# Optimization experiments

Hardware: AMD Instinct MI355X
Metric: run time of the kernel (lower is better)

The kernel has to match this reference:

```python
import jax, jax.numpy as jnp
import numpy as np

T, B, V, D, H, L, AH = 64, 128, 50000, 300, 300, 20, 300
EPS = 1e-8


def lstm_scan(x, Wih, Whh, b, h_dim):
    # x: [T, N, d_in]; PyTorch LSTM gate order i, f, g, o
    N = x.shape[1]

    def step(carry, xt):
        h, c = carry
        g = xt @ Wih.T + h @ Whh.T + b
        i, f, gg, o = jnp.split(g, 4, axis=-1)
        c = jax.nn.sigmoid(f) * c + jax.nn.sigmoid(i) * jnp.tanh(gg)
        h = jax.nn.sigmoid(o) * jnp.tanh(c)
        return (h, c), h

    init = (jnp.zeros((N, h_dim), x.dtype), jnp.zeros((N, h_dim), x.dtype))
    _, hs = jax.lax.scan(step, init, x)
    return hs  # [T, N, h_dim]


def mp_full(p, v, W):
    # p:[T,B,H], v:[B,H], W:[L,H] -> [T,B,L]; cos(W_l*p, W_l*v) via W^2 contraction
    W2 = W * W
    num = jnp.einsum('tbh,bh,lh->tbl', p, v, W2)
    pn = jnp.sqrt(jnp.einsum('tbh,lh->tbl', p * p, W2))
    vn = jnp.sqrt(jnp.einsum('bh,lh->bl', v * v, W2))
    return num / (pn * vn[None] + EPS)


def mp_elem(p, q, W):
    # p,q:[T,B,H] -> [T,B,L]
    W2 = W * W
    num = jnp.einsum('tbh,lh->tbl', p * q, W2)
    pn = jnp.sqrt(jnp.einsum('tbh,lh->tbl', p * p, W2))
    qn = jnp.sqrt(jnp.einsum('tbh,lh->tbl', q * q, W2))
    return num / (pn * qn + EPS)


def mp_pair(p, h, W):
    # p:[Tp,B,H], h:[Th,B,H] -> [Tp,Th,B,L]
    W2 = W * W
    num = jnp.einsum('tbh,sbh,lh->tsbl', p, h, W2)
    pn = jnp.sqrt(jnp.einsum('tbh,lh->tbl', p * p, W2))
    hn = jnp.sqrt(jnp.einsum('sbh,lh->sbl', h * h, W2))
    return num / (pn[:, None] * hn[None] + EPS)


def match_dir(p, h, v_full, Wf, Wm, Wa, Wma):
    full = mp_full(p, v_full, Wf)                       # full matching
    maxp = mp_pair(p, h, Wm).max(axis=1)                # maxpooling matching
    pn = p / (jnp.linalg.norm(p, axis=-1, keepdims=True) + EPS)
    hn = h / (jnp.linalg.norm(h, axis=-1, keepdims=True) + EPS)
    att = jnp.einsum('tbh,sbh->tsb', pn, hn)            # cosine attention
    w = att / (att.sum(axis=1, keepdims=True) + EPS)
    hmean = jnp.einsum('tsb,sbh->tbh', w, h)
    attm = mp_elem(p, hmean, Wa)                        # attentive matching
    idx = jnp.argmax(att, axis=1)                       # [Tp,B]
    hmax = h[idx, jnp.arange(h.shape[1])]               # [Tp,B,H]
    maxattm = mp_elem(p, hmax, Wma)                     # max-attentive matching
    return jnp.concatenate([full, maxp, attm, maxattm], axis=-1)


def multi_perspective(p_fw, p_bw, h_fw, h_bw, mp_W):
    m_fw = match_dir(p_fw, h_fw, h_fw[-1], mp_W[0], mp_W[1], mp_W[2], mp_W[3])
    m_bw = match_dir(p_bw, h_bw, h_bw[0], mp_W[4], mp_W[5], mp_W[6], mp_W[7])
    return jnp.concatenate([m_fw, m_bw], axis=-1)  # [T,B,8L]


def setup_inputs() -> dict:
    key = jax.random.key(0)
    ks = jax.random.split(key, 20)
    s = 0.05
    return {
        'premise': jax.random.randint(ks[0], (T, B), 0, V),
        'hypothesis': jax.random.randint(ks[1], (T, B), 0, V),
        'embed_W': jax.random.normal(ks[2], (V, D), jnp.float32),
        'cell_Wih': jax.random.normal(ks[3], (4 * H, D), jnp.float32) * s,
        'cell_Whh': jax.random.normal(ks[4], (4 * H, H), jnp.float32) * s,
        'cell_b': jax.random.normal(ks[5], (4 * H,), jnp.float32) * s,
        'mp_W': jax.random.normal(ks[6], (8, L, H), jnp.float32),
        'agg_Wih_f': jax.random.normal(ks[7], (4 * AH, 16 * L), jnp.float32) * s,
        'agg_Whh_f': jax.random.normal(ks[8], (4 * AH, AH), jnp.float32) * s,
        'agg_b_f': jax.random.normal(ks[9], (4 * AH,), jnp.float32) * s,
        'agg_Wih_b': jax.random.normal(ks[10], (4 * AH, 16 * L), jnp.float32) * s,
        'agg_Whh_b': jax.random.normal(ks[11], (4 * AH, AH), jnp.float32) * s,
        'agg_b_b': jax.random.normal(ks[12], (4 * AH,), jnp.float32) * s,
        'bn_gamma': jnp.ones((3, 2 * AH), jnp.float32),
        'bn_beta': jnp.zeros((3, 2 * AH), jnp.float32),
        'mlp_W1': jax.random.normal(ks[13], (2 * AH, 2 * AH), jnp.float32) * s,
        'mlp_b1': jax.random.normal(ks[14], (2 * AH,), jnp.float32) * s,
        'mlp_W2': jax.random.normal(ks[15], (2 * AH, 2 * AH), jnp.float32) * s,
        'mlp_b2': jax.random.normal(ks[16], (2 * AH,), jnp.float32) * s,
        'out_W': jax.random.normal(ks[17], (3, 2 * AH), jnp.float32) * s,
        'out_b': jax.random.normal(ks[18], (3,), jnp.float32) * s,
    }


def reference(premise, hypothesis, embed_W, cell_Wih, cell_Whh, cell_b, mp_W,
              agg_Wih_f, agg_Whh_f, agg_b_f, agg_Wih_b, agg_Whh_b, agg_b_b,
              bn_gamma, bn_beta, mlp_W1, mlp_b1, mlp_W2, mlp_b2, out_W, out_b):
    p = embed_W[premise]                      # [T,B,D]
    h = embed_W[hypothesis]                   # [T,B,D]
    comb = jnp.concatenate([p, h], axis=1)    # [T,2B,D] (premise|hypothesis along batch)
    hs_fw = lstm_scan(comb, cell_Wih, cell_Whh, cell_b, H)
    hs_bw = lstm_scan(comb[::-1], cell_Wih, cell_Whh, cell_b, H)[::-1]  # time-aligned
    p_fw, h_fw = hs_fw[:, :B], hs_fw[:, B:]
    p_bw, h_bw = hs_bw[:, :B], hs_bw[:, B:]
    m_ph = multi_perspective(p_fw, p_bw, h_fw, h_bw, mp_W)
    m_hp = multi_perspective(h_fw, h_bw, p_fw, p_bw, mp_W)
    m = jnp.concatenate([m_ph, m_hp], axis=-1)  # [T,B,16L]
    a_f = lstm_scan(m, agg_Wih_f, agg_Whh_f, agg_b_f, AH)[-1]
    a_b = lstm_scan(m[::-1], agg_Wih_b, agg_Whh_b, agg_b_b, AH)[-1]
    x = jnp.concatenate([a_f, a_b], axis=-1)    # [B, 2*AH]
    inv = np.float32(1.0 / np.sqrt(1.0 + 1e-5))  # eval-mode BN, running stats (0,1)
    bn = lambda z, i: bn_gamma[i] * z * inv + bn_beta[i]
    x = jax.nn.relu(bn(x, 0) @ mlp_W1.T + mlp_b1)
    x = jax.nn.relu(bn(x, 1) @ mlp_W2.T + mlp_b2)
    return bn(x, 2) @ out_W.T + out_b           # [B, 3]
```

## Files before the change

kernel.cpp:

```cpp
#include <hip/hip_runtime.h>
#include <cstddef>
#include <cstdint>
#include <math.h>

#define EPSF 1e-8f


typedef _Float16 half8v __attribute__((ext_vector_type(8)));
typedef float f32x4v __attribute__((ext_vector_type(4)));
union U4H8 { uint4 u; half8v h; _Float16 e[8]; };

__device__ __forceinline__ float fsig(float x) {
  float e = __expf(-x);
  return __builtin_amdgcn_rcpf(1.f + e);
}
__device__ __forceinline__ float ftanh(float x) {
  float e = __expf(-2.f * fabsf(x));
  float r = (1.f - e) * __builtin_amdgcn_rcpf(1.f + e);
  return copysignf(r, x);
}

__device__ __forceinline__ uint4 gld16(const uint4* p) {
  uint4 r;
  asm volatile("global_load_dwordx4 %0, %1, off" : "=v"(r) : "v"(p));
  return r;
}

__global__ __launch_bounds__(256) void gemm_nt128(
    const float* __restrict__ A, const float* __restrict__ B,
    const float* __restrict__ bias, float* __restrict__ C,
    int M, int N, int K)
{
  __shared__ float As[16][128];
  __shared__ float Bs[16][128];
  const int tid = threadIdx.x;
  const int tx = tid & 15, ty = tid >> 4;
  const int mbase = blockIdx.y << 7, nbase = blockIdx.x << 7;
  const int lm = tid >> 1;
  const int lk = (tid & 1) << 3;
  float acc[8][8];
#pragma unroll
  for (int i = 0; i < 8; i++)
#pragma unroll
    for (int j = 0; j < 8; j++) acc[i][j] = 0.f;

  for (int kk = 0; kk < K; kk += 16) {
    {
      int m = mbase + lm;
      const float* src = A + (size_t)m * K;
#pragma unroll
      for (int q = 0; q < 2; q++) {
        int kb = kk + lk + q * 4;
        float4 v = make_float4(0.f, 0.f, 0.f, 0.f);
        if (m < M) {
          if (kb + 4 <= K) {
            v = *(const float4*)(src + kb);
          } else {
            v.x = (kb + 0 < K) ? src[kb + 0] : 0.f;
            v.y = (kb + 1 < K) ? src[kb + 1] : 0.f;
            v.z = (kb + 2 < K) ? src[kb + 2] : 0.f;
            v.w = (kb + 3 < K) ? src[kb + 3] : 0.f;
          }
        }
        As[lk + q * 4 + 0][lm] = v.x;
        As[lk + q * 4 + 1][lm] = v.y;
        As[lk + q * 4 + 2][lm] = v.z;
        As[lk + q * 4 + 3][lm] = v.w;
      }
    }
    {
      int n = nbase + lm;
      const float* src = B + (size_t)n * K;
#pragma unroll
      for (int q = 0; q < 2; q++) {
        int kb = kk + lk + q * 4;
        float4 v = make_float4(0.f, 0.f, 0.f, 0.f);
        if (n < N) {
          if (kb + 4 <= K) {
            v = *(const float4*)(src + kb);
          } else {
            v.x = (kb + 0 < K) ? src[kb + 0] : 0.f;
            v.y = (kb + 1 < K) ? src[kb + 1] : 0.f;
            v.z = (kb + 2 < K) ? src[kb + 2] : 0.f;
            v.w = (kb + 3 < K) ? src[kb + 3] : 0.f;
          }
        }
        Bs[lk + q * 4 + 0][lm] = v.x;
        Bs[lk + q * 4 + 1][lm] = v.y;
        Bs[lk + q * 4 + 2][lm] = v.z;
        Bs[lk + q * 4 + 3][lm] = v.w;
      }
    }
    __syncthreads();
#pragma unroll
    for (int k = 0; k < 16; k++) {
      float4 a0 = *(const float4*)&As[k][ty * 8];
      float4 a1 = *(const float4*)&As[k][ty * 8 + 4];
      float4 b0 = *(const float4*)&Bs[k][tx * 8];
      float4 b1 = *(const float4*)&Bs[k][tx * 8 + 4];
      float av[8] = {a0.x, a0.y, a0.z, a0.w, a1.x, a1.y, a1.z, a1.w};
      float bv[8] = {b0.x, b0.y, b0.z, b0.w, b1.x, b1.y, b1.z, b1.w};
#pragma unroll
      for (int i = 0; i < 8; i++)
#pragma unroll
        for (int j = 0; j < 8; j++) acc[i][j] += av[i] * bv[j];
    }
    __syncthreads();
  }

#pragma unroll
  for (int i = 0; i < 8; i++) {
    int m = mbase + ty * 8 + i;
    if (m >= M) continue;
#pragma unroll
    for (int jq = 0; jq < 2; jq++) {
      int n = nbase + tx * 8 + jq * 4;
      if (n >= N) continue;
      float4 v = make_float4(acc[i][jq * 4], acc[i][jq * 4 + 1],
                             acc[i][jq * 4 + 2], acc[i][jq * 4 + 3]);
      if (bias) {
        v.x += bias[n]; v.y += bias[n + 1]; v.z += bias[n + 2]; v.w += bias[n + 3];
      }
      *(float4*)(C + (size_t)m * N + n) = v;
    }
  }
}

__global__ __launch_bounds__(256) void permW_kernel(
    const float* __restrict__ W, const float* __restrict__ bias,
    float* __restrict__ Wp, float* __restrict__ bp, int K)
{
  int r = blockIdx.x;
  int gate = r & 3, u = r >> 2;
  int src = gate * 300 + u;
  const float* s = W + (size_t)src * K;
  float* d = Wp + (size_t)r * K;
  for (int c = threadIdx.x; c < K; c += 256) d[c] = s[c];
  if (threadIdx.x == 0) bp[r] = bias[src];
}

__global__ __launch_bounds__(256) void packB_kernel(
    const float* __restrict__ W0, const float* __restrict__ W1,
    const float* __restrict__ W2,
    uint4* __restrict__ T0, uint4* __restrict__ T1, uint4* __restrict__ T2)
{
  int i = blockIdx.x * 256 + threadIdx.x;
  if (i >= 48000) return;
  const float* W = (blockIdx.y == 0) ? W0 : (blockIdx.y == 1) ? W1 : W2;
  uint4* T = (blockIdx.y == 0) ? T0 : (blockIdx.y == 1) ? T1 : T2;
  int lane = i & 63;
  int tile = i >> 6;
  int nt = tile / 10, kt = tile - nt * 10;
  int lm = lane & 15, lg = lane >> 4;
  int colp = nt * 16 + lm;
  int u = colp >> 2, gate = colp & 3;
  int n = gate * 300 + u;
  U4H8 v;
#pragma unroll
  for (int j = 0; j < 8; j++) {
    int k = kt * 32 + lg * 8 + j;
    float x = (k < 300) ? W[(size_t)n * 300 + k] : 0.f;
    v.e[j] = (_Float16)x;
  }
  T[i] = v.u;
}

#define LSTM_LDS_BYTES (5248 + 38528 + 11 * 10240)

__global__ __launch_bounds__(512, 2) void lstm_res(
    const uint4* WB0, const uint4* WB1,
    const float* __restrict__ gx0, const float* __restrict__ gx1,
    float* hist0, float* hist1,
    float* hfin,
    int NB)
{
  extern __shared__ char smem[];
  _Float16* hA8 = (_Float16*)smem;
  float* gsh = (float*)(smem + 5248);
  uint4* bls = (uint4*)(smem + 5248 + 38528);

  const int b = blockIdx.x;
  const int xcd = b & 7;
  const int grp = b >> 3;
  const int dirb = xcd >> 2;
  const int n0 = (grp * 4 + (xcd & 3)) * 8;
  const int tid = threadIdx.x;
  const int wv = tid >> 6, lane = tid & 63;
  const int lm = lane & 15, lg = lane >> 4;

  const uint4* WB = dirb ? WB1 : WB0;
  const float* gx = dirb ? gx1 : gx0;
  float* hist = dirb ? hist1 : hist0;

  U4H8 br0[10], br1[10];
  {
    const uint4* p0 = WB + (size_t)(wv * 10) * 64 + lane;
    const uint4* p1 = WB + (size_t)((wv + 8) * 10) * 64 + lane;
#pragma unroll
    for (int kt = 0; kt < 10; kt++) br0[kt].u = gld16(p0 + kt * 64);
#pragma unroll
    for (int kt = 0; kt < 10; kt++) br1[kt].u = gld16(p1 + kt * 64);
  }
  for (int e = tid; e < 7040; e += 512) bls[e] = WB[16 * 640 + e];
  for (int e = tid; e < 8 * 328; e += 512) hA8[e] = (_Float16)0.f;
  asm volatile("s_waitcnt vmcnt(0)" ::: "memory");
  __builtin_amdgcn_sched_barrier(0);
  __syncthreads();

  int gxo[5], gsho[5], hAo[5], ho[5];
  bool act[5];
#pragma unroll
  for (int q = 0; q < 5; q++) {
    int e = tid + q * 512;
    act[q] = (e < 2400);
    int m = act[q] ? (e / 300) : 0;
    int u = act[q] ? (e - m * 300) : 0;
    gxo[q] = (n0 + m) * 1200 + 4 * u;
    gsho[q] = m * 1204 + 4 * u;
    hAo[q] = m * 328 + u;
    ho[q] = (n0 + m) * 300 + u;
  }

  float crs[5] = {0.f, 0.f, 0.f, 0.f, 0.f};

  for (int t = 0; t < 64; t++) {
    const int tg = dirb ? (63 - t) : t;
    const size_t gxstep = (size_t)tg * NB * 1200;

    float4 gxv[5];
#pragma unroll
    for (int q = 0; q < 5; q++) {
      gxv[q] = make_float4(0.f, 0.f, 0.f, 0.f);
      if (act[q]) gxv[q] = *(const float4*)(gx + gxstep + gxo[q]);
    }

    uint4 bA[5], bB[5];
#pragma unroll
    for (int kt = 0; kt < 5; kt++)
      bA[kt] = WB[(size_t)((27 + wv) * 10 + kt) * 64 + lane];

    U4H8 af[10];
#pragma unroll
    for (int kt = 0; kt < 10; kt++) {
      uint4 v = make_uint4(0u, 0u, 0u, 0u);
      if (lm < 8) v = *(const uint4*)&hA8[lm * 328 + kt * 32 + lg * 8];
      af[kt].u = v;
    }

    {
      f32x4v a0 = {0.f, 0.f, 0.f, 0.f};
      f32x4v a1 = {0.f, 0.f, 0.f, 0.f};
#pragma unroll
      for (int kt = 0; kt < 5; kt++)
        a0 = __builtin_amdgcn_mfma_f32_16x16x32_f16(af[kt].h, br0[kt].h, a0, 0, 0, 0);
#pragma unroll
      for (int kt = 5; kt < 10; kt++)
        a1 = __builtin_amdgcn_mfma_f32_16x16x32_f16(af[kt].h, br0[kt].h, a1, 0, 0, 0);
      if (lg < 2) {
        int col = wv * 16 + lm;
#pragma unroll
        for (int r = 0; r < 4; r++)
          gsh[(lg * 4 + r) * 1204 + col] = a0[r] + a1[r];
      }
    }
    {
      f32x4v a0 = {0.f, 0.f, 0.f, 0.f};
      f32x4v a1 = {0.f, 0.f, 0.f, 0.f};
#pragma unroll
      for (int kt = 0; kt < 5; kt++)
        a0 = __builtin_amdgcn_mfma_f32_16x16x32_f16(af[kt].h, br1[kt].h, a0, 0, 0, 0);
#pragma unroll
      for (int kt = 5; kt < 10; kt++)
        a1 = __builtin_amdgcn_mfma_f32_16x16x32_f16(af[kt].h, br1[kt].h, a1, 0, 0, 0);
      if (lg < 2) {
        int col = (wv + 8) * 16 + lm;
#pragma unroll
        for (int r = 0; r < 4; r++)
          gsh[(lg * 4 + r) * 1204 + col] = a0[r] + a1[r];
      }
    }

#pragma unroll 1
    for (int i = 0; i < 6; i++) {
      int nt = 27 + wv + 8 * i;
#pragma unroll
      for (int kt = 0; kt < 5; kt++)
        bB[kt] = WB[(size_t)(nt * 10 + 5 + kt) * 64 + lane];
      f32x4v a0 = {0.f, 0.f, 0.f, 0.f};
#pragma unroll
      for (int kt = 0; kt < 5; kt++) {
        U4H8 bb; bb.u = bA[kt];
        a0 = __builtin_amdgcn_mfma_f32_16x16x32_f16(af[kt].h, bb.h, a0, 0, 0, 0);
      }
      if (i + 1 < 6) {
#pragma unroll
        for (int kt = 0; kt < 5; kt++)
          bA[kt] = WB[(size_t)((nt + 8) * 10 + kt) * 64 + lane];
      }
      f32x4v a1 = {0.f, 0.f, 0.f, 0.f};
#pragma unroll
      for (int kt = 0; kt < 5; kt++) {
        U4H8 bb; bb.u = bB[kt];
        a1 = __builtin_amdgcn_mfma_f32_16x16x32_f16(af[5 + kt].h, bb.h, a1, 0, 0, 0);
      }
      if (lg < 2) {
        int col = nt * 16 + lm;
#pragma unroll
        for (int r = 0; r < 4; r++)
          gsh[(lg * 4 + r) * 1204 + col] = a0[r] + a1[r];
      }
    }

#pragma unroll 1
    for (int li = 0; li < 2; li++) {
      int idxL = li == 0 ? wv : (8 + wv);
      if (li == 1 && wv >= 3) break;
      const uint4* bt = &bls[idxL * 640];
      f32x4v a0 = {0.f, 0.f, 0.f, 0.f};
      f32x4v a1 = {0.f, 0.f, 0.f, 0.f};
#pragma unroll
      for (int kt = 0; kt < 5; kt++) {
        U4H8 bb; bb.u = bt[kt * 64 + lane];
        a0 = __builtin_amdgcn_mfma_f32_16x16x32_f16(af[kt].h, bb.h, a0, 0, 0, 0);
      }
#pragma unroll
      for (int kt = 5; kt < 10; kt++) {
        U4H8 bb; bb.u = bt[kt * 64 + lane];
        a1 = __builtin_amdgcn_mfma_f32_16x16x32_f16(af[kt].h, bb.h, a1, 0, 0, 0);
      }
      if (lg < 2) {
        int col = (16 + idxL) * 16 + lm;
#pragma unroll
        for (int r = 0; r < 4; r++)
          gsh[(lg * 4 + r) * 1204 + col] = a0[r] + a1[r];
      }
    }
    __syncthreads();

#pragma unroll
    for (int q = 0; q < 5; q++) {
      if (act[q]) {
        const float4 gs = *(const float4*)&gsh[gsho[q]];
        float gi = gxv[q].x + gs.x;
        float gf = gxv[q].y + gs.y;
        float gg = gxv[q].z + gs.z;
        float go = gxv[q].w + gs.w;
        float si = fsig(gi);
        float sf = fsig(gf);
        float so = fsig(go);
        float cc = sf * crs[q] + si * ftanh(gg);
        float h = so * ftanh(cc);
        crs[q] = cc;
        hA8[hAo[q]] = (_Float16)h;
        if (hist) hist[(size_t)tg * NB * 300 + ho[q]] = h;
        if (hfin && t == 63) hfin[(size_t)dirb * NB * 300 + ho[q]] = h;
      }
    }
    __syncthreads();
  }
}

__global__ void embed_kernel(
    const int* __restrict__ prem, const int* __restrict__ hyp,
    const float* __restrict__ embW, float* __restrict__ comb)
{
  size_t i = (size_t)blockIdx.x * 256 + threadIdx.x;
  if (i >= (size_t)64 * 256 * 75) return;
  int d4 = (int)(i % 75);
  size_t r = i / 75;
  int n = (int)(r % 256);
  int t = (int)(r / 256);
  int id = (n < 128) ? prem[t * 128 + n] : hyp[t * 128 + (n - 128)];
  float4 v = *(const float4*)(embW + (size_t)id * 300 + d4 * 4);
  *(float4*)(comb + ((size_t)t * 256 + n) * 300 + d4 * 4) = v;
}

__global__ __launch_bounds__(320) void norm4_kernel(
    const float* __restrict__ hs_fw, const float* __restrict__ hs_bw,
    const float* __restrict__ mp_W,
    float* __restrict__ nm4, float* __restrict__ pnorm)
{
  const int t = blockIdx.x, n = blockIdx.y, dir = blockIdx.z;
  const float* HS = dir ? hs_bw : hs_fw;
  const float* row = HS + ((size_t)t * 256 + n) * 300;
  __shared__ float sh[300];
  const int tid = threadIdx.x, g = tid >> 4, lane = tid & 15;
  for (int k = tid; k < 300; k += 320) sh[k] = row[k];
  __syncthreads();
  if (g == 0) {
    float s2 = 0.f;
    for (int k = lane; k < 300; k += 16) { float x = sh[k]; s2 += x * x; }
    for (int o = 8; o; o >>= 1) s2 += __shfl_down(s2, o, 16);
    if (lane == 0) pnorm[((size_t)dir * 64 + t) * 256 + n] = sqrtf(s2);
  }
#pragma unroll
  for (int wset = 0; wset < 4; wset++) {
    const float* W = mp_W + dir * 24000 + wset * 6000 + g * 300;
    float s1 = 0.f;
    for (int k = lane; k < 300; k += 16) {
      float x = sh[k];
      float w = W[k];
      s1 += x * x * w * w;
    }
    for (int o = 8; o; o >>= 1) s1 += __shfl_down(s1, o, 16);
    if (lane == 0)
      nm4[((((size_t)dir * 4 + wset) * 64 + t) * 256 + n) * 20 + g] = sqrtf(s1);
  }
}

__global__ __launch_bounds__(256) void att_kernel(
    const float* __restrict__ hs_fw, const float* __restrict__ hs_bw,
    const float* __restrict__ pnorm,
    float* __restrict__ watt, int* __restrict__ idxbuf)
{
  const int b = blockIdx.x, z = blockIdx.y;
  const int dir = z & 1;
  const float* HS = dir ? hs_bw : hs_fw;
  const int p_n = (z < 2) ? b : 128 + b;
  const int h_n = (z < 2) ? 128 + b : b;
  const float* pnD = pnorm + (size_t)dir * 16384;

  __shared__ float pch[64 * 100];
  __shared__ float hch[64 * 100];
  __shared__ float att[64 * 65];
  __shared__ float winv_sh[64];

  const int tid = threadIdx.x;
  const int i = tid >> 4, j = tid & 15;
  float acc[4][4];
#pragma unroll
  for (int a = 0; a < 4; a++)
#pragma unroll
    for (int c = 0; c < 4; c++) acc[a][c] = 0.f;

  for (int kc = 0; kc < 300; kc += 100) {
    for (int e = tid; e < 1600; e += 256) {
      int row = e / 25, kq = e - row * 25;
      float4 v = *(const float4*)(HS + ((size_t)row * 256 + p_n) * 300 + kc + kq * 4);
      *(float4*)&pch[row * 100 + kq * 4] = v;
      float4 w = *(const float4*)(HS + ((size_t)row * 256 + h_n) * 300 + kc + kq * 4);
      *(float4*)&hch[row * 100 + kq * 4] = w;
    }
    __syncthreads();
#pragma unroll 5
    for (int kq = 0; kq < 25; kq++) {
      float4 av[4], bv[4];
#pragma unroll
      for (int a = 0; a < 4; a++) av[a] = *(const float4*)&pch[(i + 16 * a) * 100 + kq * 4];
#pragma unroll
      for (int c = 0; c < 4; c++) bv[c] = *(const float4*)&hch[(j + 16 * c) * 100 + kq * 4];
#pragma unroll
      for (int a = 0; a < 4; a++)
#pragma unroll
        for (int c = 0; c < 4; c++)
          acc[a][c] += av[a].x * bv[c].x + av[a].y * bv[c].y + av[a].z * bv[c].z + av[a].w * bv[c].w;
    }
    __syncthreads();
  }

#pragma unroll
  for (int a = 0; a < 4; a++) {
    int t = i + 16 * a;
    float pn = pnD[t * 256 + p_n] + EPSF;
#pragma unroll
    for (int c = 0; c < 4; c++) {
      int s = j + 16 * c;
      float hn = pnD[s * 256 + h_n] + EPSF;
      att[t * 65 + s] = acc[a][c] / (pn * hn);
    }
  }
  __syncthreads();
  if (tid < 64) {
    int t = tid;
    float ssum = 0.f, mx = -1e30f; int mi = 0;
    for (int s = 0; s < 64; s++) {
      float a = att[t * 65 + s];
      ssum += a;
      if (a > mx) { mx = a; mi = s; }
    }
    winv_sh[t] = 1.f / (ssum + EPSF);
    idxbuf[((size_t)z * 128 + b) * 64 + t] = mi;
  }
  __syncthreads();
  for (int e = tid; e < 4096; e += 256) {
    int t = e >> 6, s = e & 63;
    watt[((size_t)z * 128 + b) * 4096 + t * 64 + s] = att[t * 65 + s] * winv_sh[t];
  }
}

__global__ __launch_bounds__(256) void hmean_kernel(
    const float* __restrict__ hs_fw, const float* __restrict__ hs_bw,
    const float* __restrict__ watt, float* __restrict__ hmeanbuf)
{
  const int b = blockIdx.x, z = blockIdx.y;
  const int dir = z & 1;
  const float* HS = dir ? hs_bw : hs_fw;
  const int h_n = (z < 2) ? 128 + b : b;

  __shared__ float wsh[64 * 65];
  __shared__ float hch[64 * 128];

  const int tid = threadIdx.x;
  const int ti = tid >> 4, kj = tid & 15;
  const float* wsrc = watt + ((size_t)z * 128 + b) * 4096;
  for (int e = tid; e < 4096; e += 256) {
    int t = e >> 6, s = e & 63;
    wsh[t * 65 + s] = wsrc[t * 64 + s];
  }

  for (int kbase = 0; kbase < 300; kbase += 128) {
    int kw = min(128, 300 - kbase);
    int nf4 = kw >> 2;
    __syncthreads();
    for (int e = tid; e < 64 * nf4; e += 256) {
      int row = e / nf4, q = e - row * nf4;
      float4 v = *(const float4*)(HS + ((size_t)row * 256 + h_n) * 300 + kbase + q * 4);
      *(float4*)&hch[row * 128 + q * 4] = v;
    }
    __syncthreads();
    float acc[4][8];
#pragma unroll
    for (int a = 0; a < 4; a++)
#pragma unroll
      for (int c = 0; c < 8; c++) acc[a][c] = 0.f;
    for (int s = 0; s < 64; s++) {
      float4 h0 = *(const float4*)&hch[s * 128 + 4 * kj];
      float4 h1 = *(const float4*)&hch[s * 128 + 4 * (kj + 16)];
#pragma unroll
      for (int a = 0; a < 4; a++) {
        float w = wsh[(4 * ti + a) * 65 + s];
        acc[a][0] += w * h0.x; acc[a][1] += w * h0.y; acc[a][2] += w * h0.z; acc[a][3] += w * h0.w;
        acc[a][4] += w * h1.x; acc[a][5] += w * h1.y; acc[a][6] += w * h1.z; acc[a][7] += w * h1.w;
      }
    }
#pragma unroll
    for (int a = 0; a < 4; a++) {
      int t = 4 * ti + a;
#pragma unroll
      for (int c = 0; c < 2; c++) {
        int kq = kj + 16 * c;
        if (kq * 4 < kw) {
          int k = kbase + kq * 4;
          float4 v = make_float4(acc[a][4 * c], acc[a][4 * c + 1], acc[a][4 * c + 2], acc[a][4 * c + 3]);
          *(float4*)&hmeanbuf[(((size_t)z * 128 + b) * 64 + t) * 300 + k] = v;
        }
      }
    }
  }
}

#define MAXP_LDS_BYTES (41984 + 41984 + 13120 + 5120 + 5120)

__global__ __launch_bounds__(512, 2) void maxp_mfma(
    const float* __restrict__ hs_fw, const float* __restrict__ hs_bw,
    const float* __restrict__ mp_W, const float* __restrict__ nm4,
    float* __restrict__ m_out)
{
  extern __shared__ char smem[];
  _Float16* pA = (_Float16*)smem;
  _Float16* hB = (_Float16*)(smem + 41984);
  _Float16* w2h = (_Float16*)(smem + 83968);
  float* pn_sh = (float*)(smem + 97088);
  float* hn_sh = (float*)(smem + 102208);

  const int b = blockIdx.x, z = blockIdx.y;
  const int dir = z & 1;
  const float* HS = dir ? hs_bw : hs_fw;
  const int p_n = (z < 2) ? b : 128 + b;
  const int h_n = (z < 2) ? 128 + b : b;
  const float* Wm = mp_W + dir * 24000 + 6000;
  const float* nmD = nm4 + ((size_t)dir * 4 + 1) * 327680;

  const int tid = threadIdx.x;
  const int wv = tid >> 6, lane = tid & 63;
  const int lm = lane & 15, lg = lane >> 4;

  for (int e = tid; e < 4800; e += 512) {
    int row = e / 75, q = e - row * 75;
    float4 v = *(const float4*)(HS + ((size_t)row * 256 + p_n) * 300 + q * 4);
    float4 w = *(const float4*)(HS + ((size_t)row * 256 + h_n) * 300 + q * 4);
    _Float16* pd = &pA[row * 328 + q * 4];
    pd[0] = (_Float16)v.x; pd[1] = (_Float16)v.y; pd[2] = (_Float16)v.z; pd[3] = (_Float16)v.w;
    _Float16* hd = &hB[row * 328 + q * 4];
    hd[0] = (_Float16)w.x; hd[1] = (_Float16)w.y; hd[2] = (_Float16)w.z; hd[3] = (_Float16)w.w;
  }
  for (int e = tid; e < 64 * 28; e += 512) {
    int row = e / 28, c = 300 + (e - row * 28);
    pA[row * 328 + c] = (_Float16)0.f;
    hB[row * 328 + c] = (_Float16)0.f;
  }
  for (int e = tid; e < 1500; e += 512) {
    int row = e / 75, q = e - row * 75;
    float4 w = *(const float4*)(Wm + (size_t)row * 300 + q * 4);
    _Float16* d = &w2h[row * 328 + q * 4];
    d[0] = (_Float16)(w.x * w.x); d[1] = (_Float16)(w.y * w.y);
    d[2] = (_Float16)(w.z * w.z); d[3] = (_Float16)(w.w * w.w);
  }
  for (int e = tid; e < 20 * 28; e += 512) {
    int row = e / 28, c = 300 + (e - row * 28);
    w2h[row * 328 + c] = (_Float16)0.f;
  }
  for (int e = tid; e < 1280; e += 512) {
    int tq = e / 20, l = e - tq * 20;
    pn_sh[e] = nmD[((size_t)tq * 256 + p_n) * 20 + l];
    hn_sh[e] = nmD[((size_t)tq * 256 + h_n) * 20 + l];
  }
  __syncthreads();

  float rmax[10][4];
#pragma unroll
  for (int i = 0; i < 10; i++)
#pragma unroll
    for (int r = 0; r < 4; r++) rmax[i][r] = -1e30f;

#pragma unroll
  for (int sp = 0; sp < 2; sp++) {
    U4H8 hf[2][10];
#pragma unroll
    for (int hh = 0; hh < 2; hh++)
#pragma unroll
      for (int kt = 0; kt < 10; kt++)
        hf[hh][kt].u = *(const uint4*)&hB[(sp * 32 + hh * 16 + lm) * 328 + kt * 32 + lg * 8];

#pragma unroll
    for (int i = 0; i < 10; i++) {
      int xt = wv + 8 * i;
      int l = xt >> 2, t0 = (xt & 3) << 4;
      U4H8 af[10];
#pragma unroll
      for (int kt = 0; kt < 10; kt++) {
        U4H8 pf, wf;
        pf.u = *(const uint4*)&pA[(t0 + lm) * 328 + kt * 32 + lg * 8];
        wf.u = *(const uint4*)&w2h[l * 328 + kt * 32 + lg * 8];
        af[kt].h = pf.h * wf.h;
      }
      float pnv[4];
#pragma unroll
      for (int r = 0; r < 4; r++) pnv[r] = pn_sh[(t0 + lg * 4 + r) * 20 + l];
#pragma unroll
      for (int hh = 0; hh < 2; hh++) {
        int st = sp * 2 + hh;
        f32x4v acc = {0.f, 0.f, 0.f, 0.f};
#pragma unroll
        for (int kt = 0; kt < 10; kt++)
          acc = __builtin_amdgcn_mfma_f32_16x16x32_f16(af[kt].h, hf[hh][kt].h, acc, 0, 0, 0);
        float hn = hn_sh[(st * 16 + lm) * 20 + l];
#pragma unroll
        for (int r = 0; r < 4; r++) {
          float val = acc[r] * __builtin_amdgcn_rcpf(pnv[r] * hn + EPSF);
          rmax[i][r] = fmaxf(rmax[i][r], val);
        }
      }
    }
  }

#pragma unroll
  for (int i = 0; i < 10; i++) {
    int xt = wv + 8 * i;
    int l = xt >> 2, t0 = (xt & 3) << 4;
#pragma unroll
    for (int r = 0; r < 4; r++) {
      float v = rmax[i][r];
#pragma unroll
      for (int off = 8; off; off >>= 1) v = fmaxf(v, __shfl_down(v, off, 16));
      if (lm == 0) {
        int t = t0 + lg * 4 + r;
        m_out[((size_t)t * 128 + b) * 320 + z * 80 + 20 + l] = v;
      }
    }
  }
}

__global__ __launch_bounds__(320) void rest_kernel(
    const float* __restrict__ hs_fw, const float* __restrict__ hs_bw,
    const float* __restrict__ mp_W, const float* __restrict__ nm4,
    const float* __restrict__ hmeanbuf, const int* __restrict__ idxbuf,
    float* __restrict__ m_out)
{
  const int b = blockIdx.x, z = blockIdx.y;
  const int dir = z & 1;
  const float* HS = dir ? hs_bw : hs_fw;
  const int p_n = (z < 2) ? b : 128 + b;
  const int h_n = (z < 2) ? 128 + b : b;
  const int v_t = dir ? 0 : 63;

  __shared__ float w2f[6000], w2a[6000], w2m[6000];
  __shared__ float vsh[300], psh[300], hmsh[300], hxsh[300];

  const int tid = threadIdx.x;
  const int g = tid >> 4, lane = tid & 15;
  const float* Wf = mp_W + dir * 24000;
  const float* Wa = Wf + 12000;
  const float* Wma = Wf + 18000;
  for (int e = tid; e < 6000; e += 320) {
    float a = Wf[e], bb = Wa[e], c = Wma[e];
    w2f[e] = a * a; w2a[e] = bb * bb; w2m[e] = c * c;
  }
  for (int e = tid; e < 300; e += 320)
    vsh[e] = HS[((size_t)v_t * 256 + h_n) * 300 + e];
  __syncthreads();

  const float* base0 = nm4 + ((size_t)dir * 4 + 0) * 327680;
  const float* base2 = nm4 + ((size_t)dir * 4 + 2) * 327680;
  const float* base3 = nm4 + ((size_t)dir * 4 + 3) * 327680;
  const float vnf = base0[((size_t)v_t * 256 + h_n) * 20 + g];

  for (int t = 0; t < 64; t++) {
    int idx = idxbuf[((size_t)z * 128 + b) * 64 + t];
    __syncthreads();
    for (int e = tid; e < 300; e += 320) {
      psh[e] = HS[((size_t)t * 256 + p_n) * 300 + e];
      hmsh[e] = hmeanbuf[(((size_t)z * 128 + b) * 64 + t) * 300 + e];
      hxsh[e] = HS[((size_t)idx * 256 + h_n) * 300 + e];
    }
    __syncthreads();
    float nf = 0.f, na = 0.f, qa = 0.f, nm = 0.f;
#pragma unroll
    for (int c = 0; c < 5; c++) {
      int k4 = lane + 16 * c;
      if (k4 < 75) {
        float4 p = *(const float4*)&psh[4 * k4];
        float4 v = *(const float4*)&vsh[4 * k4];
        float4 hm = *(const float4*)&hmsh[4 * k4];
        float4 hx = *(const float4*)&hxsh[4 * k4];
        float4 wf = *(const float4*)&w2f[g * 300 + 4 * k4];
        float4 wa = *(const float4*)&w2a[g * 300 + 4 * k4];
        float4 wm = *(const float4*)&w2m[g * 300 + 4 * k4];
        nf += p.x * v.x * wf.x + p.y * v.y * wf.y + p.z * v.z * wf.z + p.w * v.w * wf.w;
        na += p.x * hm.x * wa.x + p.y * hm.y * wa.y + p.z * hm.z * wa.z + p.w * hm.w * wa.w;
        qa += hm.x * hm.x * wa.x + hm.y * hm.y * wa.y + hm.z * hm.z * wa.z + hm.w * hm.w * wa.w;
        nm += p.x * hx.x * wm.x + p.y * hx.y * wm.y + p.z * hx.z * wm.z + p.w * hx.w * wm.w;
      }
    }
#pragma unroll
    for (int o = 8; o; o >>= 1) {
      nf += __shfl_down(nf, o);
      na += __shfl_down(na, o);
      qa += __shfl_down(qa, o);
      nm += __shfl_down(nm, o);
    }
    if (lane == 0) {
      float pnf = base0[((size_t)t * 256 + p_n) * 20 + g];
      float pna = base2[((size_t)t * 256 + p_n) * 20 + g];
      float pnm = base3[((size_t)t * 256 + p_n) * 20 + g];
      float qnm = base3[((size_t)idx * 256 + h_n) * 20 + g];
      float* mrow = m_out + ((size_t)t * 128 + b) * 320 + z * 80;
      mrow[g] = nf / (pnf * vnf + EPSF);
      mrow[40 + g] = na / (pna * sqrtf(qa) + EPSF);
      mrow[60 + g] = nm / (pnm * qnm + EPSF);
    }
  }
}

__global__ __launch_bounds__(256) void mlp_kernel(
    const float* __restrict__ shA0, const float* __restrict__ shA1,
    const float* __restrict__ bnG, const float* __restrict__ bnB,
    const float* __restrict__ W1, const float* __restrict__ b1,
    const float* __restrict__ W2, const float* __restrict__ b2,
    const float* __restrict__ outW, const float* __restrict__ outb,
    float* __restrict__ out)
{
  const int b = blockIdx.x;
  const int tid = threadIdx.x;
  __shared__ float x0[600], x1[600];
  const float inv = 1.0f / sqrtf(1.0f + 1e-5f);
  for (int j = tid; j < 600; j += 256) {
    float v = (j < 300) ? shA0[b * 300 + j] : shA1[b * 300 + (j - 300)];
    x0[j] = bnG[j] * v * inv + bnB[j];
  }
  __syncthreads();
  for (int j = tid; j < 600; j += 256) {
    float acc = b1[j];
    const float* w = W1 + (size_t)j * 600;
    for (int k = 0; k < 600; k++) acc += x0[k] * w[k];
    float r = fmaxf(acc, 0.f);
    x1[j] = bnG[600 + j] * r * inv + bnB[600 + j];
  }
  __syncthreads();
  for (int j = tid; j < 600; j += 256) {
    float acc = b2[j];
    const float* w = W2 + (size_t)j * 600;
    for (int k = 0; k < 600; k++) acc += x1[k] * w[k];
    float r = fmaxf(acc, 0.f);
    x0[j] = bnG[1200 + j] * r * inv + bnB[1200 + j];
  }
  __syncthreads();
  if (tid < 3) {
    float acc = outb[tid];
    const float* w = outW + tid * 600;
    for (int k = 0; k < 600; k++) acc += x0[k] * w[k];
    out[b * 3 + tid] = acc;
  }
}

extern "C" void kernel_launch(void* const* d_in, const int* in_sizes, int n_in,
                              void* d_out, int out_size, void* d_ws, size_t ws_size,
                              hipStream_t stream) {
  const int* premise = (const int*)d_in[0];
  const int* hypothesis = (const int*)d_in[1];
  const float* embW = (const float*)d_in[2];
  const float* cWih = (const float*)d_in[3];
  const float* cWhh = (const float*)d_in[4];
  const float* cb = (const float*)d_in[5];
  const float* mpW = (const float*)d_in[6];
  const float* aWihF = (const float*)d_in[7];
  const float* aWhhF = (const float*)d_in[8];
  const float* abF = (const float*)d_in[9];
  const float* aWihB = (const float*)d_in[10];
  const float* aWhhB = (const float*)d_in[11];
  const float* abB = (const float*)d_in[12];
  const float* bnG = (const float*)d_in[13];
  const float* bnB = (const float*)d_in[14];
  const float* W1 = (const float*)d_in[15];
  const float* b1 = (const float*)d_in[16];
  const float* W2 = (const float*)d_in[17];
  const float* b2 = (const float*)d_in[18];
  const float* outW = (const float*)d_in[19];
  const float* outb = (const float*)d_in[20];
  float* out = (float*)d_out;

  float* ws = (float*)d_ws;
  float* comb  = ws + 0;
  float* gates = ws + 4915200;
  float* hsfw  = ws + 24576000;
  float* hsbw  = ws + 29491200;
  float* pnorm = ws + 34406400;
  float* mbuf  = ws + 35094528;
  float* sha   = ws + 38023168;

  uint4* WBctx = (uint4*)comb;
  uint4* WBaf  = (uint4*)(comb + 192000);
  uint4* WBab  = (uint4*)(comb + 384000);
  float* aWihFP = comb + 576000;
  float* aWihBP = comb + 960000;
  float* abFP   = comb + 1344000;
  float* abBP   = comb + 1345200;

  float* cWihP = hsfw;
  float* cbP   = hsfw + 360000;

  float* watt     = gates;
  float* hmeanbuf = gates + 2097152;
  int*   idxbuf   = (int*)(gates + 11927552);
  float* nm4      = gates + 11960320;

  hipFuncSetAttribute((const void*)lstm_res,
                      hipFuncAttributeMaxDynamicSharedMemorySize, LSTM_LDS_BYTES);
  hipFuncSetAttribute((const void*)maxp_mfma,
                      hipFuncAttributeMaxDynamicSharedMemorySize, MAXP_LDS_BYTES);

  embed_kernel<<<dim3(4800), dim3(256), 0, stream>>>(premise, hypothesis, embW, comb);
  permW_kernel<<<dim3(1200), dim3(256), 0, stream>>>(cWih, cb, cWihP, cbP, 300);

  gemm_nt128<<<dim3(10, 128), dim3(256), 0, stream>>>(comb, cWihP, cbP, gates, 16384, 1200, 300);

  packB_kernel<<<dim3(188, 3), dim3(256), 0, stream>>>(
      cWhh, aWhhF, aWhhB, WBctx, WBaf, WBab);
  permW_kernel<<<dim3(1200), dim3(256), 0, stream>>>(aWihF, abF, aWihFP, abFP, 320);
  permW_kernel<<<dim3(1200), dim3(256), 0, stream>>>(aWihB, abB, aWihBP, abBP, 320);

  lstm_res<<<dim3(64), dim3(512), LSTM_LDS_BYTES, stream>>>(
      WBctx, WBctx, gates, gates, hsfw, hsbw, nullptr, 256);

  norm4_kernel<<<dim3(64, 256, 2), dim3(320), 0, stream>>>(hsfw, hsbw, mpW, nm4, pnorm);

  att_kernel<<<dim3(128, 4), dim3(256), 0, stream>>>(hsfw, hsbw, pnorm, watt, idxbuf);
  hmean_kernel<<<dim3(128, 4), dim3(256), 0, stream>>>(hsfw, hsbw, watt, hmeanbuf);
  maxp_mfma<<<dim3(128, 4), dim3(512), MAXP_LDS_BYTES, stream>>>(
      hsfw, hsbw, mpW, nm4, mbuf);
  rest_kernel<<<dim3(128, 4), dim3(320), 0, stream>>>(hsfw, hsbw, mpW, nm4, hmeanbuf, idxbuf, mbuf);

  float* gaf = gates;
  float* gab = gates + 9830400;
  gemm_nt128<<<dim3(10, 64), dim3(256), 0, stream>>>(mbuf, aWihFP, abFP, gaf, 8192, 1200, 320);
  gemm_nt128<<<dim3(10, 64), dim3(256), 0, stream>>>(mbuf, aWihBP, abBP, gab, 8192, 1200, 320);

  lstm_res<<<dim3(32), dim3(512), LSTM_LDS_BYTES, stream>>>(
      WBaf, WBab, gaf, gab, nullptr, nullptr, sha, 128);

  mlp_kernel<<<dim3(128), dim3(256), 0, stream>>>(
      sha, sha + 38400, bnG, bnB, W1, b1, W2, b2, outW, outb, out);
}
```

Measured before the change: 2.118 ms.

## Replace FP32 SIMT input-projection GEMM with split-FP16 MFMA GEMM

```diff
diff --git a/kernel.cpp b/kernel.cpp
--- a/kernel.cpp
+++ b/kernel.cpp
@@ -26,102 +26,102 @@
   return r;
 }
 
-__global__ __launch_bounds__(256) void gemm_nt128(
+#define GMM_LDS_BYTES (2 * (128 * 72 * 2) + 2 * (240 * 72 * 2))
+
+__global__ __launch_bounds__(512, 1) void gemm_mfma_nt(
     const float* __restrict__ A, const float* __restrict__ B,
     const float* __restrict__ bias, float* __restrict__ C,
-    int M, int N, int K)
-{
-  __shared__ float As[16][128];
-  __shared__ float Bs[16][128];
+    int M, int K)
+{
+  extern __shared__ char smem[];
+  _Float16* Ah = (_Float16*)smem;
+  _Float16* Al = (_Float16*)(smem + 18432);
+  _Float16* Bh = (_Float16*)(smem + 36864);
+  _Float16* Bl = (_Float16*)(smem + 36864 + 34560);
+
   const int tid = threadIdx.x;
-  const int tx = tid & 15, ty = tid >> 4;
-  const int mbase = blockIdx.y << 7, nbase = blockIdx.x << 7;
-  const int lm = tid >> 1;
-  const int lk = (tid & 1) << 3;
-  float acc[8][8];
-#pragma unroll
-  for (int i = 0; i < 8; i++)
-#pragma unroll
-    for (int j = 0; j < 8; j++) acc[i][j] = 0.f;
-
-  for (int kk = 0; kk < K; kk += 16) {
-    {
-      int m = mbase + lm;
-      const float* src = A + (size_t)m * K;
-#pragma unroll
-      for (int q = 0; q < 2; q++) {
-        int kb = kk + lk + q * 4;
-        float4 v = make_float4(0.f, 0.f, 0.f, 0.f);
-        if (m < M) {
-          if (kb + 4 <= K) {
-            v = *(const float4*)(src + kb);
-          } else {
-            v.x = (kb + 0 < K) ? src[kb + 0] : 0.f;
-            v.y = (kb + 1 < K) ? src[kb + 1] : 0.f;
-            v.z = (kb + 2 < K) ? src[kb + 2] : 0.f;
-            v.w = (kb + 3 < K) ? src[kb + 3] : 0.f;
-          }
-        }
-        As[lk + q * 4 + 0][lm] = v.x;
-        As[lk + q * 4 + 1][lm] = v.y;
-        As[lk + q * 4 + 2][lm] = v.z;
-        As[lk + q * 4 + 3][lm] = v.w;
-      }
-    }
-    {
-      int n = nbase + lm;
-      const float* src = B + (size_t)n * K;
-#pragma unroll
-      for (int q = 0; q < 2; q++) {
-        int kb = kk + lk + q * 4;
-        float4 v = make_float4(0.f, 0.f, 0.f, 0.f);
-        if (n < N) {
-          if (kb + 4 <= K) {
-            v = *(const float4*)(src + kb);
-          } else {
-            v.x = (kb + 0 < K) ? src[kb + 0] : 0.f;
-            v.y = (kb + 1 < K) ? src[kb + 1] : 0.f;
-            v.z = (kb + 2 < K) ? src[kb + 2] : 0.f;
-            v.w = (kb + 3 < K) ? src[kb + 3] : 0.f;
-          }
-        }
-        Bs[lk + q * 4 + 0][lm] = v.x;
-        Bs[lk + q * 4 + 1][lm] = v.y;
-        Bs[lk + q * 4 + 2][lm] = v.z;
-        Bs[lk + q * 4 + 3][lm] = v.w;
-      }
-    }
-    __syncthreads();
-#pragma unroll
-    for (int k = 0; k < 16; k++) {
-      float4 a0 = *(const float4*)&As[k][ty * 8];
-      float4 a1 = *(const float4*)&As[k][ty * 8 + 4];
-      float4 b0 = *(const float4*)&Bs[k][tx * 8];
-      float4 b1 = *(const float4*)&Bs[k][tx * 8 + 4];
-      float av[8] = {a0.x, a0.y, a0.z, a0.w, a1.x, a1.y, a1.z, a1.w};
-      float bv[8] = {b0.x, b0.y, b0.z, b0.w, b1.x, b1.y, b1.z, b1.w};
-#pragma unroll
-      for (int i = 0; i < 8; i++)
-#pragma unroll
-        for (int j = 0; j < 8; j++) acc[i][j] += av[i] * bv[j];
-    }
-    __syncthreads();
-  }
-
-#pragma unroll
-  for (int i = 0; i < 8; i++) {
-    int m = mbase + ty * 8 + i;
-    if (m >= M) continue;
-#pragma unroll
-    for (int jq = 0; jq < 2; jq++) {
-      int n = nbase + tx * 8 + jq * 4;
-      if (n >= N) continue;
-      float4 v = make_float4(acc[i][jq * 4], acc[i][jq * 4 + 1],
-                             acc[i][jq * 4 + 2], acc[i][jq * 4 + 3]);
-      if (bias) {
-        v.x += bias[n]; v.y += bias[n + 1]; v.z += bias[n + 2]; v.w += bias[n + 3];
-      }
-      *(float4*)(C + (size_t)m * N + n) = v;
+  const int wv = tid >> 6, lane = tid & 63;
+  const int lm = lane & 15, lg = lane >> 4;
+  const int mbase = blockIdx.y << 7;
+  const int nbase = blockIdx.x * 240;
+
+  f32x4v acc[15];
+#pragma unroll
+  for (int nt = 0; nt < 15; nt++) acc[nt] = (f32x4v){0.f, 0.f, 0.f, 0.f};
+
+  const int nchunk = (K + 63) >> 6;
+  for (int c = 0; c < nchunk; c++) {
+    const int kc = c << 6;
+    for (int e = tid; e < 2048; e += 512) {
+      int row = e >> 4, q = e & 15;
+      int k = kc + q * 4;
+      const float* src = A + (size_t)(mbase + row) * K;
+      float4 v = make_float4(0.f, 0.f, 0.f, 0.f);
+      if (k + 4 <= K) {
+        v = *(const float4*)(src + k);
+      } else {
+        if (k + 0 < K) v.x = src[k + 0];
+        if (k + 1 < K) v.y = src[k + 1];
+        if (k + 2 < K) v.z = src[k + 2];
+        if (k + 3 < K) v.w = src[k + 3];
+      }
+      _Float16 hx = (_Float16)v.x, hy = (_Float16)v.y,
+               hz = (_Float16)v.z, hw = (_Float16)v.w;
+      _Float16* d = &Ah[row * 72 + q * 4];
+      d[0] = hx; d[1] = hy; d[2] = hz; d[3] = hw;
+      _Float16* dl = &Al[row * 72 + q * 4];
+      dl[0] = (_Float16)(v.x - (float)hx); dl[1] = (_Float16)(v.y - (float)hy);
+      dl[2] = (_Float16)(v.z - (float)hz); dl[3] = (_Float16)(v.w - (float)hw);
+    }
+    for (int e = tid; e < 3840; e += 512) {
+      int row = e >> 4, q = e & 15;
+      int k = kc + q * 4;
+      const float* src = B + (size_t)(nbase + row) * K;
+      float4 v = make_float4(0.f, 0.f, 0.f, 0.f);
+      if (k + 4 <= K) {
+        v = *(const float4*)(src + k);
+      } else {
+        if (k + 0 < K) v.x = src[k + 0];
+        if (k + 1 < K) v.y = src[k + 1];
+        if (k + 2 < K) v.z = src[k + 2];
+        if (k + 3 < K) v.w = src[k + 3];
+      }
+      _Float16 hx = (_Float16)v.x, hy = (_Float16)v.y,
+               hz = (_Float16)v.z, hw = (_Float16)v.w;
+      _Float16* d = &Bh[row * 72 + q * 4];
+      d[0] = hx; d[1] = hy; d[2] = hz; d[3] = hw;
+      _Float16* dl = &Bl[row * 72 + q * 4];
+      dl[0] = (_Float16)(v.x - (float)hx); dl[1] = (_Float16)(v.y - (float)hy);
+      dl[2] = (_Float16)(v.z - (float)hz); dl[3] = (_Float16)(v.w - (float)hw);
+    }
+    __syncthreads();
+
+#pragma unroll
+    for (int kt = 0; kt < 2; kt++) {
+      U4H8 ah, al;
+      ah.u = *(const uint4*)&Ah[(wv * 16 + lm) * 72 + kt * 32 + lg * 8];
+      al.u = *(const uint4*)&Al[(wv * 16 + lm) * 72 + kt * 32 + lg * 8];
+#pragma unroll
+      for (int nt = 0; nt < 15; nt++) {
+        U4H8 bh, bl;
+        bh.u = *(const uint4*)&Bh[(nt * 16 + lm) * 72 + kt * 32 + lg * 8];
+        bl.u = *(const uint4*)&Bl[(nt * 16 + lm) * 72 + kt * 32 + lg * 8];
+        acc[nt] = __builtin_amdgcn_mfma_f32_16x16x32_f16(ah.h, bh.h, acc[nt], 0, 0, 0);
+        acc[nt] = __builtin_amdgcn_mfma_f32_16x16x32_f16(al.h, bh.h, acc[nt], 0, 0, 0);
+        acc[nt] = __builtin_amdgcn_mfma_f32_16x16x32_f16(ah.h, bl.h, acc[nt], 0, 0, 0);
+      }
+    }
+    __syncthreads();
+  }
+
+#pragma unroll
+  for (int nt = 0; nt < 15; nt++) {
+    int col = nbase + nt * 16 + lm;
+    float bv = bias[col];
+#pragma unroll
+    for (int r = 0; r < 4; r++) {
+      int m = mbase + wv * 16 + lg * 4 + r;
+      C[(size_t)m * 1200 + col] = acc[nt][r] + bv;
     }
   }
 }
@@ -848,11 +848,14 @@
                       hipFuncAttributeMaxDynamicSharedMemorySize, LSTM_LDS_BYTES);
   hipFuncSetAttribute((const void*)maxp_mfma,
                       hipFuncAttributeMaxDynamicSharedMemorySize, MAXP_LDS_BYTES);
+  hipFuncSetAttribute((const void*)gemm_mfma_nt,
+                      hipFuncAttributeMaxDynamicSharedMemorySize, GMM_LDS_BYTES);
 
   embed_kernel<<<dim3(4800), dim3(256), 0, stream>>>(premise, hypothesis, embW, comb);
   permW_kernel<<<dim3(1200), dim3(256), 0, stream>>>(cWih, cb, cWihP, cbP, 300);
 
-  gemm_nt128<<<dim3(10, 128), dim3(256), 0, stream>>>(comb, cWihP, cbP, gates, 16384, 1200, 300);
+  gemm_mfma_nt<<<dim3(5, 128), dim3(512), GMM_LDS_BYTES, stream>>>(
+      comb, cWihP, cbP, gates, 16384, 300);
 
   packB_kernel<<<dim3(188, 3), dim3(256), 0, stream>>>(
       cWhh, aWhhF, aWhhB, WBctx, WBaf, WBab);
@@ -872,8 +875,10 @@
 
   float* gaf = gates;
   float* gab = gates + 9830400;
-  gemm_nt128<<<dim3(10, 64), dim3(256), 0, stream>>>(mbuf, aWihFP, abFP, gaf, 8192, 1200, 320);
-  gemm_nt128<<<dim3(10, 64), dim3(256), 0, stream>>>(mbuf, aWihBP, abBP, gab, 8192, 1200, 320);
+  gemm_mfma_nt<<<dim3(5, 64), dim3(512), GMM_LDS_BYTES, stream>>>(
+      mbuf, aWihFP, abFP, gaf, 8192, 320);
+  gemm_mfma_nt<<<dim3(5, 64), dim3(512), GMM_LDS_BYTES, stream>>>(
+      mbuf, aWihBP, abBP, gab, 8192, 320);
 
   lstm_res<<<dim3(32), dim3(512), LSTM_LDS_BYTES, stream>>>(
       WBaf, WBab, gaf, gab, nullptr, nullptr, sha, 128);
```

Result: faster. 1.980 ms (median of 2 runs) (-6.5%).
